# Kernel tuning notes

Hardware: AMD Instinct MI355X
Metric: run time of the kernel (lower is better)

## Reference

```python
import jax, jax.numpy as jnp
import numpy as np

A, B, D, H = 64, 256, 128, 512  # seq rows, columns (encoder batch / decode loop), n_dims, hidden


def _lstm_step(Wih, Whh, bih, bhh, h, c, x):
    # x: [N, D], h/c: [N, H]; PyTorch gate order i, f, g, o
    gates = x @ Wih.T + bih + h @ Whh.T + bhh  # [N, 4H]
    i, f, g, o = jnp.split(gates, 4, axis=-1)
    c = jax.nn.sigmoid(f) * c + jax.nn.sigmoid(i) * jnp.tanh(g)
    h = jax.nn.sigmoid(o) * jnp.tanh(c)
    return h, c


def setup_inputs() -> dict:
    key = jax.random.key(0)
    ks = jax.random.split(key, 12)
    s = 0.05
    inp = {
        "input_tensor": jax.random.normal(ks[0], (A, B, D), jnp.float32),
        "enc_Wih": jax.random.normal(ks[1], (4 * H, D), jnp.float32) * s,
        "enc_Whh": jax.random.normal(ks[2], (4 * H, H), jnp.float32) * s,
        "enc_bih": jax.random.normal(ks[3], (4 * H,), jnp.float32) * s,
        "enc_bhh": jax.random.normal(ks[4], (4 * H,), jnp.float32) * s,
        "dec_Wih": jax.random.normal(ks[5], (4 * H, D), jnp.float32) * s,
        "dec_Whh": jax.random.normal(ks[6], (4 * H, H), jnp.float32) * s,
        "dec_bih": jax.random.normal(ks[7], (4 * H,), jnp.float32) * s,
        "dec_bhh": jax.random.normal(ks[8], (4 * H,), jnp.float32) * s,
        "lin_W": jax.random.normal(ks[9], (D, H), jnp.float32) * s,
        "lin_b": jax.random.normal(ks[10], (D,), jnp.float32) * s,
    }
    return inp


def reference(input_tensor, enc_Wih, enc_Whh, enc_bih, enc_bhh,
              dec_Wih, dec_Whh, dec_bih, dec_bhh, lin_W, lin_b):
    a, b, d = input_tensor.shape
    h_dim = enc_Whh.shape[1]
    dt = input_tensor.dtype

    # ---- encoder: seq-first LSTM over dim0 (len a), batch = b ----
    def e_step(hc, x_t):
        h, c = hc
        h, c = _lstm_step(enc_Wih, enc_Whh, enc_bih, enc_bhh, h, c, x_t)
        return (h, c), None

    h0 = jnp.zeros((b, h_dim), dt)
    (hN, cN), _ = jax.lax.scan(e_step, (h0, h0), input_tensor)
    # hidden[0][:, -1].unsqueeze(1): keep only the LAST batch element -> [1, H]
    dh, dc = hN[-1:], cN[-1:]

    # ---- decoder: loop i = b-1 .. 0; emit linear(h) then run length-a LSTM on column i ----
    def col_step(hc, x_col):  # x_col: [a, d]
        h, c = hc
        out_i = (h @ lin_W.T + lin_b)[0]  # [d], emitted BEFORE processing the column

        def t_step(hc2, x_t):
            h2, c2 = hc2
            h2, c2 = _lstm_step(dec_Wih, dec_Whh, dec_bih, dec_bhh, h2, c2, x_t[None])
            return (h2, c2), None

        (h, c), _ = jax.lax.scan(t_step, (h, c), x_col)
        return (h, c), out_i

    x_cols = jnp.flip(jnp.transpose(input_tensor, (1, 0, 2)), 0)  # [b, a, d], reversed i
    _, outs = jax.lax.scan(col_step, (dh, dc), x_cols)  # [b, d] in reversed order
    outs = jnp.flip(outs, 0)
    # outputs[:, i, :] = [1, d] row broadcast across all a rows
    return jnp.broadcast_to(outs[None, :, :], (a, b, d))
```

## Files before the change

### kernel.cpp

```cpp
#include <hip/hip_runtime.h>
#include <math.h>

#define A_ 64
#define B_ 256
#define D_ 128
#define H_ 512
#define STEPS_ENC 64
#define STEPS_TOT (64 + 16384)
#define NWG 32

#define XCC_GETREG_IMM (20 | (31 << 11))

#define OFF_XT    0
#define N_XT      (A_*D_*B_)
#define OFF_HT0   (OFF_XT + N_XT)
#define OFF_HT1   (OFF_HT0 + H_*B_)
#define OFF_CT    (OFF_HT1 + H_*B_)
#define OFF_HTAP  (OFF_CT + H_*B_)
#define OFF_HB64  (OFF_HTAP + B_*H_)
#define OFF_CINIT (OFF_HB64 + 4*H_)
#define OFF_ELECT (OFF_CINIT + H_)

__device__ __forceinline__ float tanhfast(float x) {
  return 1.0f - 2.0f * __builtin_amdgcn_rcpf(__expf(2.0f * x) + 1.0f);
}

__device__ __forceinline__ unsigned long long load_nt(const unsigned long long* p) {
  unsigned long long v;
  asm volatile("global_load_dwordx2 %0, %1, off nt\n\ts_waitcnt vmcnt(0)"
               : "=&v"(v) : "v"(p) : "memory");
  return v;
}
__device__ __forceinline__ unsigned long long load_inv(const unsigned long long* p) {
  unsigned long long v;
  asm volatile("buffer_inv sc0\n\t"
               "global_load_dwordx2 %0, %1, off nt\n\ts_waitcnt vmcnt(0)"
               : "=&v"(v) : "v"(p) : "memory");
  return v;
}
__device__ __forceinline__ void store_nt(unsigned long long* p, unsigned long long v) {
  asm volatile("global_store_dwordx2 %0, %1, off nt" :: "v"(p), "v"(v) : "memory");
}

__global__ void init0(float* __restrict__ ws) {
  unsigned long long* HB = (unsigned long long*)(ws + OFF_HB64);
  int* EL = (int*)(ws + OFF_ELECT);
  int j = threadIdx.x;
  HB[H_ + j] = 0ull;
  HB[j]      = 0xFFFFFFFF00000000ull;
  if (j < 8) EL[j] = 0;
  if (j == 8) EL[8] = -1;
}

template<int PHASE>
__device__ __forceinline__ void lstm_phase(
    const float* __restrict__ in0,
    const float* __restrict__ Wih, const float* __restrict__ Whh,
    const float* __restrict__ bih, const float* __restrict__ bhh,
    unsigned long long* __restrict__ HB, float* __restrict__ HTAP,
    float (*part)[16 * 64], float* hstage,
    int w, int v, int l, float& c,
    float actA, float actB, float actC)
{
  const int R = ((l >> 4) << 9) + (w << 4) + (l & 15);

  float4 wa[8];
#pragma unroll
  for (int k = 0; k < 8; ++k)
    wa[k] = *(const float4*)&Whh[R * H_ + (v << 5) + 4 * k];
  float4 wx0 = *(const float4*)&Wih[R * D_ + (v << 3)];
  float4 wx1 = *(const float4*)&Wih[R * D_ + (v << 3) + 4];

  float bias = 0.f;
  if (v == 0) bias = bih[R] + bhh[R];

  const int pe = (v << 5) + (l & 31);

  const int s0 = (PHASE == 0) ? 0 : STEPS_ENC;
  const int s1 = (PHASE == 0) ? STEPS_ENC : STEPS_TOT;

  for (int s = s0; s < s1; ++s) {
    const float* xp;
    if (PHASE == 0) {
      xp = in0 + (s * B_ + 255) * D_ + (v << 3);
    } else {
      const int sd = s - STEPS_ENC;
      const int tt = sd & 63;
      const int bc = 255 - (sd >> 6);
      xp = in0 + (tt * B_ + bc) * D_ + (v << 3);
    }
    float4 x0 = *(const float4*)xp;
    float4 x1 = *(const float4*)(xp + 4);

    unsigned long long* slot = &HB[(((s + 1) & 1) << 9) + pe];
    unsigned long long pk;
    int spins = 0;
    for (;;) {
      pk = ((++spins & 63) == 0) ? load_inv(slot) : load_nt(slot);
      if (__all((unsigned)(pk >> 32) == (unsigned)s)) break;
    }
    if (l < 32) hstage[pe] = __uint_as_float((unsigned)pk);

    float p = wx0.x * x0.x + wx0.y * x0.y + wx0.z * x0.z + wx0.w * x0.w
            + wx1.x * x1.x + wx1.y * x1.y + wx1.z * x1.z + wx1.w * x1.w;

    const float4* hp = (const float4*)&hstage[v << 5];
#pragma unroll
    for (int k = 0; k < 8; ++k) {
      float4 h4 = hp[k];
      p += wa[k].x * h4.x + wa[k].y * h4.y + wa[k].z * h4.z + wa[k].w * h4.w;
    }
    part[s & 1][(v << 6) + l] = p;
    __syncthreads();

    if (v == 0) {
      float g = bias;
#pragma unroll
      for (int j = 0; j < 16; ++j) g += part[s & 1][(j << 6) + l];
      float a = fmaf(actA,
                     __builtin_amdgcn_rcpf(__expf(actB * g) + 1.0f), actC);
      const int e = l & 15;
      float ai = __shfl(a, e);
      float af = __shfl(a, e + 16);
      float ag = __shfl(a, e + 32);
      float ao = __shfl(a, e + 48);
      if (l < 16) {
        c = af * c + ai * ag;
        float hn = ao * tanhfast(c);
        if ((s & 63) == 63) {
          int q = s >> 6;
          if (q < 256) HTAP[q * H_ + (w << 4) + l] = hn;
        }
        unsigned long long opk =
            ((unsigned long long)(unsigned)(s + 1) << 32) | __float_as_uint(hn);
        store_nt(&HB[((s & 1) << 9) + (w << 4) + l], opk);
      }
    }
  }
}

__global__ __launch_bounds__(1024) void fused(
    const float* __restrict__ in0,
    const float* __restrict__ eWih, const float* __restrict__ eWhh,
    const float* __restrict__ ebih, const float* __restrict__ ebhh,
    const float* __restrict__ dWih, const float* __restrict__ dWhh,
    const float* __restrict__ dbih, const float* __restrict__ dbhh,
    float* __restrict__ ws)
{
  unsigned long long* HB = (unsigned long long*)(ws + OFF_HB64);
  float* HTAP = ws + OFF_HTAP;

  __shared__ float part[2][16 * 64];
  __shared__ float hstage[H_];
  __shared__ int role;

  const int tid = threadIdx.x;

  if (tid == 0) {
    unsigned xcc = ((unsigned)__builtin_amdgcn_s_getreg(XCC_GETREG_IMM)) & 7u;
    int* EL = (int*)(ws + OFF_ELECT);
    int r = __hip_atomic_fetch_add(&EL[xcc], 1, __ATOMIC_RELAXED,
                                   __HIP_MEMORY_SCOPE_AGENT);
    int myrole = -1;
    if (r < NWG) {
      if (r == NWG - 1) {
        int exp = -1;
        __hip_atomic_compare_exchange_strong(&EL[8], &exp, (int)xcc,
            __ATOMIC_RELAXED, __ATOMIC_RELAXED, __HIP_MEMORY_SCOPE_AGENT);
      }
      int wx;
      do {
        wx = __hip_atomic_load(&EL[8], __ATOMIC_RELAXED, __HIP_MEMORY_SCOPE_AGENT);
        if (wx == -1) __builtin_amdgcn_s_sleep(2);
      } while (wx == -1);
      if (wx == (int)xcc) myrole = r;
    }
    role = myrole;
  }
  __syncthreads();
  if (role < 0) return;
  const int w = role;

  const int v = tid >> 6;
  const int l = tid & 63;

  const int gate = l >> 4;
  const float actA = (gate == 2) ? -2.0f :  1.0f;
  const float actB = (gate == 2) ?  2.0f : -1.0f;
  const float actC = (gate == 2) ?  1.0f :  0.0f;

  float c = 0.f;

  lstm_phase<0>(in0, eWih, eWhh, ebih, ebhh, HB, HTAP, part, hstage,
                w, v, l, c, actA, actB, actC);
  lstm_phase<1>(in0, dWih, dWhh, dbih, dbhh, HB, HTAP, part, hstage,
                w, v, l, c, actA, actB, actC);
}

__global__ __launch_bounds__(128) void out_proj(
    const float* __restrict__ ws, const float* __restrict__ linW,
    const float* __restrict__ linb, float* __restrict__ out) {
  const float* HTAP = ws + OFF_HTAP;
  __shared__ float hs[H_];
  const int b = blockIdx.x;
  const int i = 255 - b;
  const int d = threadIdx.x;
  *(float4*)&hs[4 * d] = *(const float4*)&HTAP[i * H_ + 4 * d];
  __syncthreads();
  float acc = linb[d];
#pragma unroll 8
  for (int k = 0; k < H_; k += 4) {
    float4 w4 = *(const float4*)&linW[d * H_ + k];
    acc += w4.x * hs[k] + w4.y * hs[k + 1] + w4.z * hs[k + 2] + w4.w * hs[k + 3];
  }
  for (int a = 0; a < A_; ++a)
    out[(a * B_ + b) * D_ + d] = acc;
}

extern "C" void kernel_launch(void* const* d_in, const int* in_sizes, int n_in,
                              void* d_out, int out_size, void* d_ws, size_t ws_size,
                              hipStream_t stream) {
  const float* in0  = (const float*)d_in[0];
  const float* eWih = (const float*)d_in[1];
  const float* eWhh = (const float*)d_in[2];
  const float* ebih = (const float*)d_in[3];
  const float* ebhh = (const float*)d_in[4];
  const float* dWih = (const float*)d_in[5];
  const float* dWhh = (const float*)d_in[6];
  const float* dbih = (const float*)d_in[7];
  const float* dbhh = (const float*)d_in[8];
  const float* linW = (const float*)d_in[9];
  const float* linb = (const float*)d_in[10];
  float* ws = (float*)d_ws;
  float* out = (float*)d_out;

  init0<<<1, 512, 0, stream>>>(ws);
  fused<<<256, 1024, 0, stream>>>(in0, eWih, eWhh, ebih, ebhh,
                                  dWih, dWhh, dbih, dbhh, ws);
  out_proj<<<256, 128, 0, stream>>>(ws, linW, linb, out);
}
```

Measured before the change: 19.81 ms.

## Remap LSTM work so each wave owns one hidden unit, reduce via DPP

Each of the 16 waves per workgroup now computes all four gates for a single hidden unit, with the 16 lanes of each gate row splitting the K dimension. The partial sums are combined with DPP row rotations instead of being written to shared memory and summed by wave 0 after a barrier. This removes the second shared-memory round trip and the serialized gate epilogue in wave 0, leaving one barrier per step that sits before the h dot product. The shared h buffer is double-buffered and padded to avoid bank conflicts; every wave now runs the activation math redundantly.

New measurement: 18.61 ms. 6.1% less time.

```diff
diff --git a/kernel.cpp b/kernel.cpp
--- a/kernel.cpp
+++ b/kernel.cpp
@@ -42,6 +42,22 @@
   asm volatile("global_store_dwordx2 %0, %1, off nt" :: "v"(p), "v"(v) : "memory");
 }
 
+template<int CTRL>
+__device__ __forceinline__ float dpp_ror_add(float x) {
+  int y = __builtin_amdgcn_update_dpp(0, __float_as_int(x), CTRL, 0xF, 0xF, false);
+  return x + __int_as_float(y);
+}
+__device__ __forceinline__ float row_allsum16(float x) {
+  x = dpp_ror_add<0x128>(x);
+  x = dpp_ror_add<0x124>(x);
+  x = dpp_ror_add<0x122>(x);
+  x = dpp_ror_add<0x121>(x);
+  return x;
+}
+
+#define HSP 36
+#define HS_N (16 * HSP)
+
 __global__ void init0(float* __restrict__ ws) {
   unsigned long long* HB = (unsigned long long*)(ws + OFF_HB64);
   int* EL = (int*)(ws + OFF_ELECT);
@@ -58,21 +74,22 @@
     const float* __restrict__ Wih, const float* __restrict__ Whh,
     const float* __restrict__ bih, const float* __restrict__ bhh,
     unsigned long long* __restrict__ HB, float* __restrict__ HTAP,
-    float (*part)[16 * 64], float* hstage,
+    float* hstage,
     int w, int v, int l, float& c,
     float actA, float actB, float actC)
 {
-  const int R = ((l >> 4) << 9) + (w << 4) + (l & 15);
-
-  float4 wa[8];
+  const int g = l >> 4;
+  const int j = l & 15;
+  const int u = (w << 4) + v;
+  const int R = (g << 9) + u;
+
+  float4 wh[8];
 #pragma unroll
   for (int k = 0; k < 8; ++k)
-    wa[k] = *(const float4*)&Whh[R * H_ + (v << 5) + 4 * k];
-  float4 wx0 = *(const float4*)&Wih[R * D_ + (v << 3)];
-  float4 wx1 = *(const float4*)&Wih[R * D_ + (v << 3) + 4];
-
-  float bias = 0.f;
-  if (v == 0) bias = bih[R] + bhh[R];
+    wh[k] = *(const float4*)&Whh[R * H_ + (j << 5) + (k << 2)];
+  float4 wx0 = *(const float4*)&Wih[R * D_ + (j << 3)];
+  float4 wx1 = *(const float4*)&Wih[R * D_ + (j << 3) + 4];
+  const float bias = (j == 0) ? (bih[R] + bhh[R]) : 0.f;
 
   const int pe = (v << 5) + (l & 31);
 
@@ -82,15 +99,13 @@
   for (int s = s0; s < s1; ++s) {
     const float* xp;
     if (PHASE == 0) {
-      xp = in0 + (s * B_ + 255) * D_ + (v << 3);
+      xp = in0 + (s * B_ + 255) * D_;
     } else {
       const int sd = s - STEPS_ENC;
-      const int tt = sd & 63;
-      const int bc = 255 - (sd >> 6);
-      xp = in0 + (tt * B_ + bc) * D_ + (v << 3);
-    }
-    float4 x0 = *(const float4*)xp;
-    float4 x1 = *(const float4*)(xp + 4);
+      xp = in0 + ((sd & 63) * B_ + (255 - (sd >> 6))) * D_;
+    }
+    float4 x0 = *(const float4*)(xp + (j << 3));
+    float4 x1 = *(const float4*)(xp + (j << 3) + 4);
 
     unsigned long long* slot = &HB[(((s + 1) & 1) << 9) + pe];
     unsigned long long pk;
@@ -99,42 +114,38 @@
       pk = ((++spins & 63) == 0) ? load_inv(slot) : load_nt(slot);
       if (__all((unsigned)(pk >> 32) == (unsigned)s)) break;
     }
-    if (l < 32) hstage[pe] = __uint_as_float((unsigned)pk);
-
-    float p = wx0.x * x0.x + wx0.y * x0.y + wx0.z * x0.z + wx0.w * x0.w
-            + wx1.x * x1.x + wx1.y * x1.y + wx1.z * x1.z + wx1.w * x1.w;
-
-    const float4* hp = (const float4*)&hstage[v << 5];
+    float* hbuf = hstage + (s & 1) * HS_N;
+    if (l < 32) hbuf[(v * HSP) + (l & 31)] = __uint_as_float((unsigned)pk);
+
+    float acc = bias
+              + wx0.x * x0.x + wx0.y * x0.y + wx0.z * x0.z + wx0.w * x0.w
+              + wx1.x * x1.x + wx1.y * x1.y + wx1.z * x1.z + wx1.w * x1.w;
+
+    __syncthreads();
+
+    const float4* hp = (const float4*)&hbuf[j * HSP];
 #pragma unroll
     for (int k = 0; k < 8; ++k) {
       float4 h4 = hp[k];
-      p += wa[k].x * h4.x + wa[k].y * h4.y + wa[k].z * h4.z + wa[k].w * h4.w;
-    }
-    part[s & 1][(v << 6) + l] = p;
-    __syncthreads();
-
-    if (v == 0) {
-      float g = bias;
-#pragma unroll
-      for (int j = 0; j < 16; ++j) g += part[s & 1][(j << 6) + l];
-      float a = fmaf(actA,
-                     __builtin_amdgcn_rcpf(__expf(actB * g) + 1.0f), actC);
-      const int e = l & 15;
-      float ai = __shfl(a, e);
-      float af = __shfl(a, e + 16);
-      float ag = __shfl(a, e + 32);
-      float ao = __shfl(a, e + 48);
-      if (l < 16) {
-        c = af * c + ai * ag;
-        float hn = ao * tanhfast(c);
-        if ((s & 63) == 63) {
-          int q = s >> 6;
-          if (q < 256) HTAP[q * H_ + (w << 4) + l] = hn;
-        }
-        unsigned long long opk =
-            ((unsigned long long)(unsigned)(s + 1) << 32) | __float_as_uint(hn);
-        store_nt(&HB[((s & 1) << 9) + (w << 4) + l], opk);
+      acc += wh[k].x * h4.x + wh[k].y * h4.y + wh[k].z * h4.z + wh[k].w * h4.w;
+    }
+
+    float a = row_allsum16(acc);
+    a = fmaf(actA, __builtin_amdgcn_rcpf(__expf(actB * a) + 1.0f), actC);
+    float ai = __shfl(a, 0);
+    float af = __shfl(a, 16);
+    float ag = __shfl(a, 32);
+    float ao = __shfl(a, 48);
+    c = af * c + ai * ag;
+    float hn = ao * tanhfast(c);
+    if (l == 0) {
+      if ((s & 63) == 63) {
+        int q = s >> 6;
+        if (q < 256) HTAP[q * H_ + u] = hn;
       }
+      unsigned long long opk =
+          ((unsigned long long)(unsigned)(s + 1) << 32) | __float_as_uint(hn);
+      store_nt(&HB[((s & 1) << 9) + u], opk);
     }
   }
 }
@@ -150,8 +161,7 @@
   unsigned long long* HB = (unsigned long long*)(ws + OFF_HB64);
   float* HTAP = ws + OFF_HTAP;
 
-  __shared__ float part[2][16 * 64];
-  __shared__ float hstage[H_];
+  __shared__ __align__(16) float hstage[2][HS_N];
   __shared__ int role;
 
   const int tid = threadIdx.x;
@@ -191,9 +201,9 @@
 
   float c = 0.f;
 
-  lstm_phase<0>(in0, eWih, eWhh, ebih, ebhh, HB, HTAP, part, hstage,
+  lstm_phase<0>(in0, eWih, eWhh, ebih, ebhh, HB, HTAP, &hstage[0][0],
                 w, v, l, c, actA, actB, actC);
-  lstm_phase<1>(in0, dWih, dWhh, dbih, dbhh, HB, HTAP, part, hstage,
+  lstm_phase<1>(in0, dWih, dWhh, dbih, dbhh, HB, HTAP, &hstage[0][0],
                 w, v, l, c, actA, actB, actC);
 }
 
```
